# Optimization experiments

Measured on AMD Instinct MI355X. Metric: run time of the kernel, lower is better.

## Reference

```python
import jax, jax.numpy as jnp
import numpy as np

B, L, D, NH = 4, 1024, 1024, 16
DH = D // NH
H = 8 * D // 3  # SwiGLU hidden = 2730
NEG = -1e9


def setup_inputs() -> dict:
    key = jax.random.key(0)
    ks = jax.random.split(key, 8)
    init = lambda k, shape: (jax.random.normal(k, shape, jnp.float32) * 0.02)
    x = jax.random.normal(ks[0], (B, L, D), jnp.float32)
    causal = jnp.tril(jnp.ones((L, L), bool))
    m = jnp.where(causal, 0.0, NEG)[None, None].astype(jnp.float32)  # [1,1,L,L]
    return {
        'x': x,
        'm': m,
        'wx': init(ks[1], (D, 3 * D)),
        'bx': jnp.zeros((3 * D,), jnp.float32),
        'wo': init(ks[2], (D, D)),
        'bo': jnp.zeros((D,), jnp.float32),
        'mhanorm_w': jnp.ones((D,), jnp.float32),
        'ffnorm_w': jnp.ones((D,), jnp.float32),
        'u': init(ks[3], (D, H)),
        'v': init(ks[4], (D, H)),
        'w': init(ks[5], (H, D)),
    }


def rmsnorm(x, weight, eps=1e-8):
    rrms = jax.lax.rsqrt(jnp.mean(x * x, axis=-1, keepdims=True) + eps)
    return weight * x * rrms


def reference(x, m, wx, bx, wo, bo, mhanorm_w, ffnorm_w, u, v, w):
    scale = D ** (-0.5)  # note: original uses d**-0.5, NOT dh**-0.5
    qkv = rmsnorm(x, mhanorm_w) @ wx + bx                 # [B,L,3D]
    q, k, vv = jnp.split(qkv, 3, axis=-1)                  # each [B,L,D]
    split = lambda t: t.reshape(B, L, NH, DH).transpose(0, 2, 1, 3)  # [B,NH,L,DH]
    q, k, vv = split(q), split(k), split(vv)               # pe = identity (default)
    scores = jnp.einsum('bhic,bhjc->bhij', q, k) * scale + m
    A = jax.nn.softmax(scores, axis=-1)
    head = jnp.einsum('bhij,bhjc->bhic', A, vv)            # [B,NH,L,DH]
    head = head.transpose(0, 2, 1, 3).reshape(B, L, D)
    x = x + head @ wo + bo
    xn = rmsnorm(x, ffnorm_w)
    return x + (jax.nn.silu(xn @ u) * (xn @ v)) @ w
```

## Files before the change

kernel.cpp:

```cpp
#include <hip/hip_runtime.h>

#define B_  4
#define L_  1024
#define D_  1024
#define NH_ 16
#define DH_ 64
#define H_  2730
#define HP_ 2816
#define M_  4096

typedef short bf16x8 __attribute__((ext_vector_type(8)));
typedef float f32x4  __attribute__((ext_vector_type(4)));

__device__ __forceinline__ unsigned short f2bf(float f) {
    unsigned int u = __builtin_bit_cast(unsigned int, f);
    u += 0x7fffu + ((u >> 16) & 1u);
    return (unsigned short)(u >> 16);
}
__device__ __forceinline__ float bf2f(unsigned short s) {
    unsigned int u = ((unsigned int)s) << 16;
    return __builtin_bit_cast(float, u);
}

__device__ __forceinline__ void glds16(const void* g, void* l) {
    __builtin_amdgcn_global_load_lds(
        (const __attribute__((address_space(1))) unsigned int*)g,
        (__attribute__((address_space(3))) unsigned int*)l, 16, 0, 0);
}

__global__ __launch_bounds__(256) void cvtT_kernel(
    const float* __restrict__ in, unsigned short* __restrict__ out,
    int K, int N, int Kp, int Np)
{
    __shared__ float t[32][33];
    const int k0 = blockIdx.x * 32, n0 = blockIdx.y * 32;
    const int tx = threadIdx.x & 31, ty = threadIdx.x >> 5;
    #pragma unroll
    for (int i = 0; i < 4; ++i) {
        const int k = k0 + ty + i * 8, n = n0 + tx;
        t[ty + i * 8][tx] = (k < K && n < N) ? in[(size_t)k * N + n] : 0.0f;
    }
    __syncthreads();
    #pragma unroll
    for (int i = 0; i < 4; ++i) {
        const int n = n0 + ty + i * 8, k = k0 + tx;
        out[(size_t)n * Kp + k] = f2bf(t[tx][ty + i * 8]);
    }
}

__global__ __launch_bounds__(256) void rmsnorm_kernel(
    const float* __restrict__ x, const float* __restrict__ w,
    unsigned short* __restrict__ out)
{
    const int row = blockIdx.x;
    const int t = threadIdx.x;
    const float4 v = ((const float4*)(x + (size_t)row * 1024))[t];
    float ss = v.x*v.x + v.y*v.y + v.z*v.z + v.w*v.w;
    #pragma unroll
    for (int off = 32; off > 0; off >>= 1) ss += __shfl_down(ss, off);
    __shared__ float red[4];
    if ((t & 63) == 0) red[t >> 6] = ss;
    __syncthreads();
    const float tot = red[0] + red[1] + red[2] + red[3];
    const float rr = rsqrtf(tot * (1.0f / 1024.0f) + 1e-8f);
    const float4 wv = ((const float4*)w)[t];
    ushort4 o;
    o.x = f2bf(v.x * wv.x * rr); o.y = f2bf(v.y * wv.y * rr);
    o.z = f2bf(v.z * wv.z * rr); o.w = f2bf(v.w * wv.w * rr);
    ((ushort4*)(out + (size_t)row * 1024))[t] = o;
}

template<int EPI, int TN>
__global__ __launch_bounds__(256) void gemm_bf16(
    const unsigned short* __restrict__ A, const unsigned short* __restrict__ Bt,
    int M, int N, int K,
    const float* __restrict__ bias, const float* __restrict__ res,
    const unsigned short* __restrict__ mul,
    float* __restrict__ outf, unsigned short* __restrict__ outb)
{
    constexpr int NS = TN / 32;
    constexpr int G  = (TN == 128) ? 4 : 3;
    constexpr int WAIT_G = 0xF70 | G;
    __shared__ __align__(16) unsigned short As[2][128 * 32];
    __shared__ __align__(16) unsigned short Bs[2][TN * 32];
    const int tid = threadIdx.x;
    const int m0 = blockIdx.y * 128, n0 = blockIdx.x * TN;
    const int lane = tid & 63, w = tid >> 6;
    const int wm = w >> 1, wn = w & 1;
    const int quad = lane >> 4, l15 = lane & 15;

    f32x4 acc[4][NS] = {};

    const int p0 = w * 64 + lane;
    const int r0 = p0 >> 2, c0 = (p0 & 3) ^ (r0 & 3);
    const int offL0 = p0 * 8, offL1 = 2048 + p0 * 8;

    const unsigned short* Ag0 = A + (size_t)(m0 + r0) * K + c0 * 8;
    const unsigned short* Ag1 = A + (size_t)(m0 + 64 + r0) * K + c0 * 8;
    const unsigned short* Bg0 = Bt + (size_t)(n0 + r0) * K + c0 * 8;
    const unsigned short* Bg1 = Bt + (size_t)(n0 + 64 + r0) * K + c0 * 8;

    auto stage = [&](int kk, int buf) {
        glds16(Ag0 + kk, &As[buf][offL0]);
        glds16(Ag1 + kk, &As[buf][offL1]);
        glds16(Bg0 + kk, &Bs[buf][offL0]);
        if (TN == 128) glds16(Bg1 + kk, &Bs[buf][offL1]);
    };
    auto compute = [&](int buf) {
        bf16x8 af[4], bfr[NS];
        #pragma unroll
        for (int ms = 0; ms < 4; ++ms) {
            const int row = wm * 64 + ms * 16 + l15;
            af[ms] = *(const bf16x8*)&As[buf][row * 32 + ((quad ^ (row & 3)) * 8)];
        }
        #pragma unroll
        for (int ns = 0; ns < NS; ++ns) {
            const int row = wn * (TN / 2) + ns * 16 + l15;
            bfr[ns] = *(const bf16x8*)&Bs[buf][row * 32 + ((quad ^ (row & 3)) * 8)];
        }
        #pragma unroll
        for (int ms = 0; ms < 4; ++ms)
            #pragma unroll
            for (int ns = 0; ns < NS; ++ns)
                acc[ms][ns] = __builtin_amdgcn_mfma_f32_16x16x32_bf16(
                    af[ms], bfr[ns], acc[ms][ns], 0, 0, 0);
    };

    const int nk = K >> 5;
    stage(0, 0);
    for (int i = 0; i < nk; i += 2) {
        if (i + 1 < nk) { stage((i + 1) << 5, 1); __builtin_amdgcn_s_waitcnt(WAIT_G); }
        else            { __builtin_amdgcn_s_waitcnt(0xF70); }
        __builtin_amdgcn_s_barrier();
        compute(0);
        __builtin_amdgcn_s_barrier();
        if (i + 2 < nk) { stage((i + 2) << 5, 0); __builtin_amdgcn_s_waitcnt(WAIT_G); }
        else            { __builtin_amdgcn_s_waitcnt(0xF70); }
        __builtin_amdgcn_s_barrier();
        compute(1);
        __builtin_amdgcn_s_barrier();
    }

    #pragma unroll
    for (int ms = 0; ms < 4; ++ms) {
        #pragma unroll
        for (int r = 0; r < 4; ++r) {
            const int row = m0 + wm * 64 + ms * 16 + quad * 4 + r;
            const size_t ro = (size_t)row * N;
            #pragma unroll
            for (int ns = 0; ns < NS; ++ns) {
                const int col = n0 + wn * (TN / 2) + ns * 16 + l15;
                float v = acc[ms][ns][r];
                if (EPI == 0) {
                    outb[ro + col] = f2bf(v + bias[col]);
                } else if (EPI == 1) {
                    outf[ro + col] = v + bias[col] + res[ro + col];
                } else if (EPI == 2) {
                    outb[ro + col] = f2bf(v);
                } else if (EPI == 3) {
                    float t = bf2f(mul[ro + col]);
                    float g = v / (1.0f + __expf(-v)) * t;
                    outb[ro + col] = f2bf(g);
                } else {
                    outf[ro + col] = v + res[ro + col];
                }
            }
        }
    }
}

__global__ __launch_bounds__(256) void attn_mfma2_kernel(
    const unsigned short* __restrict__ qkv, unsigned short* __restrict__ hout)
{
    __shared__ __align__(16) unsigned short Qs[2][64 * 72];
    __shared__ __align__(16) unsigned short Ks[2][64 * 64];
    __shared__ __align__(16) unsigned short Vt[2][64 * 72];
    __shared__ __align__(16) unsigned short Ps[64 * 68];

    const int tid = threadIdx.x;
    const int qa = blockIdx.x, h = blockIdx.y, b = blockIdx.z;
    const int qb = 15 - qa;
    const int w = tid >> 6, lane = tid & 63;
    const int quad = lane >> 4, l15 = lane & 15;

    const size_t basek = (size_t)(b * L_) * 3072 + 1024 + h * 64;
    const size_t basev = basek + 1024;

    {
        const int row = tid >> 1, half = tid & 1;
        const int tile = row >> 6, r6 = row & 63;
        const int grow = (tile ? qb : qa) * 64 + r6;
        const unsigned short* gp = qkv + (size_t)(b * L_ + grow) * 3072 + h * 64 + half * 32;
        uint4 a = *(const uint4*)gp;
        uint4 c = *(const uint4*)(gp + 8);
        uint4 d = *(const uint4*)(gp + 16);
        uint4 e = *(const uint4*)(gp + 24);
        unsigned short* dp = &Qs[tile][r6 * 72 + half * 32];
        *(uint4*)dp = a; *(uint4*)(dp + 8) = c; *(uint4*)(dp + 16) = d; *(uint4*)(dp + 24) = e;
    }

    auto stageK = [&](int kt, int buf) {
        #pragma unroll
        for (int i = 0; i < 2; ++i) {
            const int p = i * 256 + tid;
            const int row = p >> 3;
            const int cc = (p & 7) ^ (row & 7);
            glds16(qkv + basek + (size_t)(kt * 64 + row) * 3072 + cc * 8, &Ks[buf][p * 8]);
        }
    };
    const int vkey = (tid & 31) * 2, vdp = tid >> 5;
    auto loadV = [&](int kt, uint4& v0, uint4& v1) {
        const unsigned short* gp = qkv + basev + (size_t)(kt * 64 + vkey) * 3072 + vdp * 8;
        v0 = *(const uint4*)gp;
        v1 = *(const uint4*)(gp + 3072);
    };
    auto writeV = [&](int buf, const uint4& v0, const uint4& v1) {
        union { uint4 u; unsigned short s[8]; } a, c;
        a.u = v0; c.u = v1;
        #pragma unroll
        for (int i = 0; i < 8; ++i) {
            unsigned int pk = (unsigned int)a.s[i] | ((unsigned int)c.s[i] << 16);
            *(unsigned int*)&Vt[buf][(vdp * 8 + i) * 72 + vkey] = pk;
        }
    };

    f32x4 O[4] = {};
    float m4[4], l4[4];
    #pragma unroll
    for (int r = 0; r < 4; ++r) { m4[r] = -1e30f; l4[r] = 0.0f; }

    stageK(0, 0);
    {
        uint4 v0, v1;
        loadV(0, v0, v1);
        writeV(0, v0, v1);
    }
    __syncthreads();

    bf16x8 af[2];
    #pragma unroll
    for (int s = 0; s < 2; ++s)
        af[s] = *(const bf16x8*)&Qs[0][(w * 16 + l15) * 72 + s * 32 + quad * 8];

    int qsel = 0, kt = 0;
    for (int t = 0; t < 17; ++t) {
        const int cb = t & 1, nb = cb ^ 1;
        const bool havenext = (t < 16);
        uint4 nv0, nv1;
        if (havenext) {
            const int ktn = (t + 1 <= qa) ? (t + 1) : (t - qa);
            stageK(ktn, nb);
            loadV(ktn, nv0, nv1);
        }

        bf16x8 bfk[4][2];
        #pragma unroll
        for (int n = 0; n < 4; ++n) {
            const int row = n * 16 + l15;
            #pragma unroll
            for (int s = 0; s < 2; ++s)
                bfk[n][s] = *(const bf16x8*)&Ks[cb][row * 64 + (((s * 4 + quad) ^ (row & 7)) * 8)];
        }
        f32x4 sacc[4] = {};
        #pragma unroll
        for (int n = 0; n < 4; ++n) {
            sacc[n] = __builtin_amdgcn_mfma_f32_16x16x32_bf16(af[0], bfk[n][0], sacc[n], 0, 0, 0);
            sacc[n] = __builtin_amdgcn_mfma_f32_16x16x32_bf16(af[1], bfk[n][1], sacc[n], 0, 0, 0);
        }

        const bool diag = (kt == (qsel ? qb : qa));
        float p[4][4], mx[4];
        #pragma unroll
        for (int r = 0; r < 4; ++r) mx[r] = -1e30f;
        #pragma unroll
        for (int n = 0; n < 4; ++n) {
            const int col = n * 16 + l15;
            #pragma unroll
            for (int r = 0; r < 4; ++r) {
                float v = sacc[n][r] * 0.03125f;
                if (diag && col > (w * 16 + quad * 4 + r)) v = -1e30f;
                p[n][r] = v;
                mx[r] = fmaxf(mx[r], v);
            }
        }
        #pragma unroll
        for (int r = 0; r < 4; ++r) {
            #pragma unroll
            for (int m = 1; m < 16; m <<= 1)
                mx[r] = fmaxf(mx[r], __shfl_xor(mx[r], m));
        }
        float alpha[4], rs[4];
        #pragma unroll
        for (int r = 0; r < 4; ++r) {
            const float mnew = fmaxf(m4[r], mx[r]);
            alpha[r] = __expf(m4[r] - mnew);
            m4[r] = mnew;
            float s0 = 0.0f;
            #pragma unroll
            for (int n = 0; n < 4; ++n) {
                const float e = __expf(p[n][r] - mnew);
                p[n][r] = e;
                s0 += e;
            }
            rs[r] = s0;
        }
        #pragma unroll
        for (int r = 0; r < 4; ++r) {
            #pragma unroll
            for (int m = 1; m < 16; m <<= 1)
                rs[r] += __shfl_xor(rs[r], m);
            l4[r] = l4[r] * alpha[r] + rs[r];
        }
        #pragma unroll
        for (int dn = 0; dn < 4; ++dn)
            #pragma unroll
            for (int r = 0; r < 4; ++r)
                O[dn][r] *= alpha[r];
        #pragma unroll
        for (int n = 0; n < 4; ++n)
            #pragma unroll
            for (int r = 0; r < 4; ++r)
                Ps[(w * 16 + quad * 4 + r) * 68 + n * 16 + l15] = f2bf(p[n][r]);

        if (havenext) writeV(nb, nv0, nv1);

        bf16x8 ap[2], bv[4][2];
        #pragma unroll
        for (int s = 0; s < 2; ++s)
            ap[s] = *(const bf16x8*)&Ps[(w * 16 + l15) * 68 + s * 32 + quad * 8];
        #pragma unroll
        for (int dn = 0; dn < 4; ++dn)
            #pragma unroll
            for (int s = 0; s < 2; ++s)
                bv[dn][s] = *(const bf16x8*)&Vt[cb][(dn * 16 + l15) * 72 + s * 32 + quad * 8];
        #pragma unroll
        for (int dn = 0; dn < 4; ++dn) {
            O[dn] = __builtin_amdgcn_mfma_f32_16x16x32_bf16(ap[0], bv[dn][0], O[dn], 0, 0, 0);
            O[dn] = __builtin_amdgcn_mfma_f32_16x16x32_bf16(ap[1], bv[dn][1], O[dn], 0, 0, 0);
        }

        if (t == qa) {
            #pragma unroll
            for (int r = 0; r < 4; ++r) {
                const float inv = 1.0f / l4[r];
                const int grow = qa * 64 + w * 16 + quad * 4 + r;
                unsigned short* op = hout + (size_t)(b * L_ + grow) * 1024 + h * 64;
                #pragma unroll
                for (int dn = 0; dn < 4; ++dn)
                    op[dn * 16 + l15] = f2bf(O[dn][r] * inv);
            }
            #pragma unroll
            for (int dn = 0; dn < 4; ++dn)
                #pragma unroll
                for (int r = 0; r < 4; ++r) O[dn][r] = 0.0f;
            #pragma unroll
            for (int r = 0; r < 4; ++r) { m4[r] = -1e30f; l4[r] = 0.0f; }
            qsel = 1;
            kt = 0;
            #pragma unroll
            for (int s = 0; s < 2; ++s)
                af[s] = *(const bf16x8*)&Qs[1][(w * 16 + l15) * 72 + s * 32 + quad * 8];
        } else {
            ++kt;
        }
        __syncthreads();
    }

    #pragma unroll
    for (int r = 0; r < 4; ++r) {
        const float inv = 1.0f / l4[r];
        const int grow = qb * 64 + w * 16 + quad * 4 + r;
        unsigned short* op = hout + (size_t)(b * L_ + grow) * 1024 + h * 64;
        #pragma unroll
        for (int dn = 0; dn < 4; ++dn)
            op[dn * 16 + l15] = f2bf(O[dn][r] * inv);
    }
}

extern "C" void kernel_launch(void* const* d_in, const int* in_sizes, int n_in,
                              void* d_out, int out_size, void* d_ws, size_t ws_size,
                              hipStream_t stream)
{
    const float* x   = (const float*)d_in[0];
    const float* wx  = (const float*)d_in[2];
    const float* bx  = (const float*)d_in[3];
    const float* wo  = (const float*)d_in[4];
    const float* bo  = (const float*)d_in[5];
    const float* mhw = (const float*)d_in[6];
    const float* ffw = (const float*)d_in[7];
    const float* u   = (const float*)d_in[8];
    const float* v   = (const float*)d_in[9];
    const float* w   = (const float*)d_in[10];
    float* out = (float*)d_out;

    char* W = (char*)d_ws;
    unsigned short* xn_bf   = (unsigned short*)(W + 0);
    unsigned short* wx_bf   = (unsigned short*)(W + 8388608);
    unsigned short* qkv_bf  = (unsigned short*)(W + 14680064);
    unsigned short* head_bf = (unsigned short*)(W + 39845888);
    unsigned short* wo_bf   = (unsigned short*)(W + 48234496);
    float*          x2      = (float*)(W + 50331648);
    unsigned short* u_bf    = (unsigned short*)(W + 67108864);
    unsigned short* v_bf    = (unsigned short*)(W + 72876032);
    unsigned short* w_bf    = (unsigned short*)(W + 78643200);
    unsigned short* g_bf    = (unsigned short*)(W + 84410368);
    unsigned short* tv_bf   = qkv_bf;

    cvtT_kernel<<<dim3(32, 96), 256, 0, stream>>>(wx, wx_bf, 1024, 3072, 1024, 3072);
    cvtT_kernel<<<dim3(32, 32), 256, 0, stream>>>(wo, wo_bf, 1024, 1024, 1024, 1024);
    cvtT_kernel<<<dim3(32, 88), 256, 0, stream>>>(u,  u_bf, 1024, 2730, 1024, 2816);
    cvtT_kernel<<<dim3(32, 88), 256, 0, stream>>>(v,  v_bf, 1024, 2730, 1024, 2816);
    cvtT_kernel<<<dim3(88, 32), 256, 0, stream>>>(w,  w_bf, 2730, 1024, 2816, 1024);

    rmsnorm_kernel<<<4096, 256, 0, stream>>>(x, mhw, xn_bf);

    gemm_bf16<0, 128><<<dim3(3072 / 128, 32), 256, 0, stream>>>(
        xn_bf, wx_bf, 4096, 3072, 1024, bx, nullptr, nullptr, nullptr, qkv_bf);

    attn_mfma2_kernel<<<dim3(8, 16, 4), 256, 0, stream>>>(qkv_bf, head_bf);

    gemm_bf16<1, 64><<<dim3(1024 / 64, 32), 256, 0, stream>>>(
        head_bf, wo_bf, 4096, 1024, 1024, bo, x, nullptr, x2, nullptr);

    rmsnorm_kernel<<<4096, 256, 0, stream>>>(x2, ffw, xn_bf);

    gemm_bf16<2, 128><<<dim3(2816 / 128, 32), 256, 0, stream>>>(
        xn_bf, v_bf, 4096, 2816, 1024, nullptr, nullptr, nullptr, nullptr, tv_bf);

    gemm_bf16<3, 128><<<dim3(2816 / 128, 32), 256, 0, stream>>>(
        xn_bf, u_bf, 4096, 2816, 1024, nullptr, nullptr, tv_bf, nullptr, g_bf);

    gemm_bf16<4, 64><<<dim3(1024 / 64, 32), 256, 0, stream>>>(
        g_bf, w_bf, 4096, 1024, 2816, nullptr, x2, nullptr, out, nullptr);
}
```

Measured before the change: 364.1 us.

## Fuse SwiGLU up/gate GEMMs into one kernel and add XCD-aware block swizzle

Replaces the two separate GEMMs for xn@v and xn@u, along with the bf16 intermediate they pass between them, with a single kernel. That kernel loads each A tile once, keeps dual accumulators for U and V, and applies silu(u)*v in the epilogue. This removes one read of the activation matrix and the intermediate write/read round trip, at the cost of doubled accumulator registers and larger shared memory per block. It also remaps block indices so that consecutive blocks on the same XCD share row tiles, aiming to improve L2 locality in all GEMMs.

```diff
diff --git a/kernel.cpp b/kernel.cpp
--- a/kernel.cpp
+++ b/kernel.cpp
@@ -26,6 +26,14 @@
     __builtin_amdgcn_global_load_lds(
         (const __attribute__((address_space(1))) unsigned int*)g,
         (__attribute__((address_space(3))) unsigned int*)l, 16, 0, 0);
+}
+
+__device__ __forceinline__ void xcd_swz(int& lx, int& ly) {
+    const int gx = gridDim.x;
+    const int flat = blockIdx.x + gx * blockIdx.y;
+    const int r = flat & 7, q = flat >> 3;
+    lx = q % gx;
+    ly = r + 8 * (q / gx);
 }
 
 __global__ __launch_bounds__(256) void cvtT_kernel(
@@ -75,7 +83,6 @@
     const unsigned short* __restrict__ A, const unsigned short* __restrict__ Bt,
     int M, int N, int K,
     const float* __restrict__ bias, const float* __restrict__ res,
-    const unsigned short* __restrict__ mul,
     float* __restrict__ outf, unsigned short* __restrict__ outb)
 {
     constexpr int NS = TN / 32;
@@ -84,7 +91,9 @@
     __shared__ __align__(16) unsigned short As[2][128 * 32];
     __shared__ __align__(16) unsigned short Bs[2][TN * 32];
     const int tid = threadIdx.x;
-    const int m0 = blockIdx.y * 128, n0 = blockIdx.x * TN;
+    int lx, ly;
+    xcd_swz(lx, ly);
+    const int m0 = ly * 128, n0 = lx * TN;
     const int lane = tid & 63, w = tid >> 6;
     const int wm = w >> 1, wn = w & 1;
     const int quad = lane >> 4, l15 = lane & 15;
@@ -155,15 +164,100 @@
                     outb[ro + col] = f2bf(v + bias[col]);
                 } else if (EPI == 1) {
                     outf[ro + col] = v + bias[col] + res[ro + col];
-                } else if (EPI == 2) {
-                    outb[ro + col] = f2bf(v);
-                } else if (EPI == 3) {
-                    float t = bf2f(mul[ro + col]);
-                    float g = v / (1.0f + __expf(-v)) * t;
-                    outb[ro + col] = f2bf(g);
                 } else {
                     outf[ro + col] = v + res[ro + col];
                 }
+            }
+        }
+    }
+}
+
+__global__ __launch_bounds__(256, 2) void gemm_swiglu(
+    const unsigned short* __restrict__ A, const unsigned short* __restrict__ Bu,
+    const unsigned short* __restrict__ Bv, unsigned short* __restrict__ g)
+{
+    constexpr int K = 1024, N = HP_;
+    constexpr int WAIT_G = 0xF76;
+    __shared__ __align__(16) unsigned short As[2][128 * 32];
+    __shared__ __align__(16) unsigned short Us[2][128 * 32];
+    __shared__ __align__(16) unsigned short Vs[2][128 * 32];
+    const int tid = threadIdx.x;
+    int lx, ly;
+    xcd_swz(lx, ly);
+    const int m0 = ly * 128, n0 = lx * 128;
+    const int lane = tid & 63, w = tid >> 6;
+    const int wm = w >> 1, wn = w & 1;
+    const int quad = lane >> 4, l15 = lane & 15;
+
+    f32x4 au[4][4] = {}, av[4][4] = {};
+
+    const int p0 = w * 64 + lane;
+    const int r0 = p0 >> 2, c0 = (p0 & 3) ^ (r0 & 3);
+    const int offL0 = p0 * 8, offL1 = 2048 + p0 * 8;
+
+    const unsigned short* Ag0 = A  + (size_t)(m0 + r0) * K + c0 * 8;
+    const unsigned short* Ag1 = A  + (size_t)(m0 + 64 + r0) * K + c0 * 8;
+    const unsigned short* Ug0 = Bu + (size_t)(n0 + r0) * K + c0 * 8;
+    const unsigned short* Ug1 = Bu + (size_t)(n0 + 64 + r0) * K + c0 * 8;
+    const unsigned short* Vg0 = Bv + (size_t)(n0 + r0) * K + c0 * 8;
+    const unsigned short* Vg1 = Bv + (size_t)(n0 + 64 + r0) * K + c0 * 8;
+
+    auto stage = [&](int kk, int buf) {
+        glds16(Ag0 + kk, &As[buf][offL0]);
+        glds16(Ag1 + kk, &As[buf][offL1]);
+        glds16(Ug0 + kk, &Us[buf][offL0]);
+        glds16(Ug1 + kk, &Us[buf][offL1]);
+        glds16(Vg0 + kk, &Vs[buf][offL0]);
+        glds16(Vg1 + kk, &Vs[buf][offL1]);
+    };
+    auto compute = [&](int buf) {
+        bf16x8 af[4], uf[4], vf[4];
+        #pragma unroll
+        for (int ms = 0; ms < 4; ++ms) {
+            const int row = wm * 64 + ms * 16 + l15;
+            af[ms] = *(const bf16x8*)&As[buf][row * 32 + ((quad ^ (row & 3)) * 8)];
+        }
+        #pragma unroll
+        for (int ns = 0; ns < 4; ++ns) {
+            const int row = wn * 64 + ns * 16 + l15;
+            uf[ns] = *(const bf16x8*)&Us[buf][row * 32 + ((quad ^ (row & 3)) * 8)];
+            vf[ns] = *(const bf16x8*)&Vs[buf][row * 32 + ((quad ^ (row & 3)) * 8)];
+        }
+        #pragma unroll
+        for (int ms = 0; ms < 4; ++ms)
+            #pragma unroll
+            for (int ns = 0; ns < 4; ++ns) {
+                au[ms][ns] = __builtin_amdgcn_mfma_f32_16x16x32_bf16(af[ms], uf[ns], au[ms][ns], 0, 0, 0);
+                av[ms][ns] = __builtin_amdgcn_mfma_f32_16x16x32_bf16(af[ms], vf[ns], av[ms][ns], 0, 0, 0);
+            }
+    };
+
+    stage(0, 0);
+    for (int i = 0; i < 32; i += 2) {
+        if (i + 1 < 32) { stage((i + 1) << 5, 1); __builtin_amdgcn_s_waitcnt(WAIT_G); }
+        else            { __builtin_amdgcn_s_waitcnt(0xF70); }
+        __builtin_amdgcn_s_barrier();
+        compute(0);
+        __builtin_amdgcn_s_barrier();
+        if (i + 2 < 32) { stage((i + 2) << 5, 0); __builtin_amdgcn_s_waitcnt(WAIT_G); }
+        else            { __builtin_amdgcn_s_waitcnt(0xF70); }
+        __builtin_amdgcn_s_barrier();
+        compute(1);
+        __builtin_amdgcn_s_barrier();
+    }
+
+    #pragma unroll
+    for (int ms = 0; ms < 4; ++ms) {
+        #pragma unroll
+        for (int r = 0; r < 4; ++r) {
+            const int row = m0 + wm * 64 + ms * 16 + quad * 4 + r;
+            const size_t ro = (size_t)row * N;
+            #pragma unroll
+            for (int ns = 0; ns < 4; ++ns) {
+                const int col = n0 + wn * 64 + ns * 16 + l15;
+                const float uu = au[ms][ns][r];
+                const float vv = av[ms][ns][r];
+                g[ro + col] = f2bf(uu / (1.0f + __expf(-uu)) * vv);
             }
         }
     }
@@ -404,7 +498,6 @@
     unsigned short* v_bf    = (unsigned short*)(W + 72876032);
     unsigned short* w_bf    = (unsigned short*)(W + 78643200);
     unsigned short* g_bf    = (unsigned short*)(W + 84410368);
-    unsigned short* tv_bf   = qkv_bf;
 
     cvtT_kernel<<<dim3(32, 96), 256, 0, stream>>>(wx, wx_bf, 1024, 3072, 1024, 3072);
     cvtT_kernel<<<dim3(32, 32), 256, 0, stream>>>(wo, wo_bf, 1024, 1024, 1024, 1024);
@@ -415,21 +508,17 @@
     rmsnorm_kernel<<<4096, 256, 0, stream>>>(x, mhw, xn_bf);
 
     gemm_bf16<0, 128><<<dim3(3072 / 128, 32), 256, 0, stream>>>(
-        xn_bf, wx_bf, 4096, 3072, 1024, bx, nullptr, nullptr, nullptr, qkv_bf);
+        xn_bf, wx_bf, 4096, 3072, 1024, bx, nullptr, nullptr, qkv_bf);
 
     attn_mfma2_kernel<<<dim3(8, 16, 4), 256, 0, stream>>>(qkv_bf, head_bf);
 
     gemm_bf16<1, 64><<<dim3(1024 / 64, 32), 256, 0, stream>>>(
-        head_bf, wo_bf, 4096, 1024, 1024, bo, x, nullptr, x2, nullptr);
+        head_bf, wo_bf, 4096, 1024, 1024, bo, x, x2, nullptr);
 
     rmsnorm_kernel<<<4096, 256, 0, stream>>>(x2, ffw, xn_bf);
 
-    gemm_bf16<2, 128><<<dim3(2816 / 128, 32), 256, 0, stream>>>(
-        xn_bf, v_bf, 4096, 2816, 1024, nullptr, nullptr, nullptr, nullptr, tv_bf);
-
-    gemm_bf16<3, 128><<<dim3(2816 / 128, 32), 256, 0, stream>>>(
-        xn_bf, u_bf, 4096, 2816, 1024, nullptr, nullptr, tv_bf, nullptr, g_bf);
+    gemm_swiglu<<<dim3(2816 / 128, 32), 256, 0, stream>>>(xn_bf, u_bf, v_bf, g_bf);
 
     gemm_bf16<4, 64><<<dim3(1024 / 64, 32), 256, 0, stream>>>(
-        g_bf, w_bf, 4096, 1024, 2816, nullptr, x2, nullptr, out, nullptr);
-}
+        g_bf, w_bf, 4096, 1024, 2816, nullptr, x2, out, nullptr);
+}
```

After: 360.1 us. No clear change (-1.1%).
